# Optimization experiments

Measured on AMD Instinct MI355X. Metric: run time of the kernel, lower is better.

Reference implementation:

```python
import jax, jax.numpy as jnp
import numpy as np

B, D, P, K_ROUTE = 131072, 256, 16, 4


def setup_inputs() -> dict:
    key = jax.random.key(0)
    ks = jax.random.split(key, 12)
    w_scale = 0.02
    return {
        "z_n": jax.random.normal(ks[0], (B, D), dtype=jnp.float32),
        "z_sea": jax.random.normal(ks[1], (B, D), dtype=jnp.float32),
        "z_trend": jax.random.normal(ks[2], (B, D), dtype=jnp.float32),
        "noise_z": jax.random.normal(ks[3], (B, D), dtype=jnp.float32),   # randn_like(z_fused)
        "noise_r": jax.random.normal(ks[4], (B, P), dtype=jnp.float32),   # randn_like(routing_logits)
        "patch_candidates": jax.random.randint(ks[5], (P,), 1, 64, dtype=jnp.int32),
        "W_proj": jax.random.normal(ks[6], (D, 3 * D), dtype=jnp.float32) * w_scale,
        "b_proj": jnp.zeros((D,), dtype=jnp.float32),
        "W_route": jax.random.normal(ks[7], (P, D), dtype=jnp.float32) * w_scale,
        "b_route": jnp.zeros((P,), dtype=jnp.float32),
        "W_noise": jax.random.normal(ks[8], (P, D), dtype=jnp.float32) * w_scale,
        "b_noise": jnp.zeros((P,), dtype=jnp.float32),
    }


def reference(z_n, z_sea, z_trend, noise_z, noise_r, patch_candidates,
              W_proj, b_proj, W_route, b_route, W_noise, b_noise):
    # feature fusion: Linear(3D -> D) on concat
    z_concat = jnp.concatenate([z_n, z_sea, z_trend], axis=-1)        # [B, 3D]
    z_fused = z_concat @ W_proj.T + b_proj                            # [B, D]
    gating_input = z_fused + noise_z * 0.1                            # noise injection 1
    routing_logits = gating_input @ W_route.T + b_route               # [B, P]
    noise_scale = jax.nn.softplus(gating_input @ W_noise.T + b_noise)  # [B, P]
    routing_logits = routing_logits + noise_r * noise_scale           # noise injection 2
    routing_weights = jax.nn.softmax(routing_logits, axis=-1)         # [B, P]
    top_k_values, top_k_indices = jax.lax.top_k(routing_weights, K_ROUTE)  # [B, K]
    rows = jnp.arange(routing_weights.shape[0])[:, None]
    sparse_routing = jnp.zeros_like(routing_weights).at[rows, top_k_indices].set(top_k_values)
    selected_patches = patch_candidates[top_k_indices]                # [B, K]
    return (sparse_routing, selected_patches, top_k_indices)
```

## Files before the change

kernel.cpp:

```cpp
#include <hip/hip_runtime.h>
#include <math.h>

#define B_ROWS 131072
#define ROWS 128
#define XP 36
#define MP 36
#define LP 34

__global__ void precompute_M(const float* __restrict__ Wp,
                             const float* __restrict__ Wr,
                             const float* __restrict__ Wn,
                             const float* __restrict__ bp,
                             const float* __restrict__ br,
                             const float* __restrict__ bn,
                             float* __restrict__ M,
                             float* __restrict__ c) {
  int o = blockIdx.x * 256 + threadIdx.x;
  if (o < 32 * 1024) {
    int j = o >> 10, k = o & 1023;
    const float* W = (j < 16) ? Wr : Wn;
    int jj = j & 15;
    float v;
    if (k < 768) {
      double s = 0.0;
      for (int d = 0; d < 256; ++d)
        s += (double)W[jj * 256 + d] * (double)Wp[d * 768 + k];
      v = (float)s;
    } else {
      v = 0.1f * W[jj * 256 + (k - 768)];
    }
    M[o] = v;
  }
  if (blockIdx.x == 0 && threadIdx.x < 32) {
    int j = threadIdx.x, jj = j & 15;
    const float* W = (j < 16) ? Wr : Wn;
    const float* b = (j < 16) ? br : bn;
    double s = (double)b[jj];
    for (int d = 0; d < 256; ++d)
      s += (double)W[jj * 256 + d] * (double)bp[d];
    c[j] = (float)s;
  }
}

__global__ __launch_bounds__(256, 3)
void router_main(const float* __restrict__ zn, const float* __restrict__ zs,
                 const float* __restrict__ zt, const float* __restrict__ nz,
                 const float* __restrict__ nr, const int* __restrict__ patches,
                 const float* __restrict__ M, const float* __restrict__ c,
                 float* __restrict__ out) {
  __shared__ float Xs[ROWS * XP];
  __shared__ float Ms[32 * MP];
  __shared__ float Ls[ROWS * LP];
  const int t = threadIdx.x;
  const int row0 = blockIdx.x * ROWS;
  const int jg = t & 7;
  const int rg = t >> 3;
  const int sr = t >> 3;
  const int sk4 = t & 7;

  float accf[4][4];
  double accd[4][4];
#pragma unroll
  for (int a = 0; a < 4; ++a)
#pragma unroll
    for (int b = 0; b < 4; ++b) { accf[a][b] = 0.f; accd[a][b] = 0.0; }

  for (int s = 0; s < 32; ++s) {
    const int k0 = s * 32;
    const float* src; int col0;
    if (k0 < 256)      { src = zn; col0 = k0; }
    else if (k0 < 512) { src = zs; col0 = k0 - 256; }
    else if (k0 < 768) { src = zt; col0 = k0 - 512; }
    else               { src = nz; col0 = k0 - 768; }

    float4 xg[4];
#pragma unroll
    for (int i = 0; i < 4; ++i)
      xg[i] = *(const float4*)&src[(size_t)(row0 + sr + 32 * i) * 256 + col0 + 4 * sk4];
    float4 mg = *(const float4*)&M[(size_t)(t >> 3) * 1024 + k0 + 4 * sk4];

    __syncthreads();
#pragma unroll
    for (int i = 0; i < 4; ++i)
      *(float4*)&Xs[(sr + 32 * i) * XP + 4 * sk4] = xg[i];
    *(float4*)&Ms[(t >> 3) * MP + 4 * sk4] = mg;
    __syncthreads();

#pragma unroll
    for (int ks = 0; ks < 8; ++ks) {
      const int k = 4 * ks;
      float4 m4[4], x4[4];
#pragma unroll
      for (int jj = 0; jj < 4; ++jj)
        m4[jj] = *(const float4*)&Ms[(jg + 8 * jj) * MP + k];
#pragma unroll
      for (int rr = 0; rr < 4; ++rr)
        x4[rr] = *(const float4*)&Xs[(rg + 32 * rr) * XP + k];
#pragma unroll
      for (int jj = 0; jj < 4; ++jj)
#pragma unroll
        for (int rr = 0; rr < 4; ++rr) {
          accf[jj][rr] += m4[jj].x * x4[rr].x;
          accf[jj][rr] += m4[jj].y * x4[rr].y;
          accf[jj][rr] += m4[jj].z * x4[rr].z;
          accf[jj][rr] += m4[jj].w * x4[rr].w;
        }
    }
#pragma unroll
    for (int jj = 0; jj < 4; ++jj)
#pragma unroll
      for (int rr = 0; rr < 4; ++rr) { accd[jj][rr] += (double)accf[jj][rr]; accf[jj][rr] = 0.f; }
  }

#pragma unroll
  for (int jj = 0; jj < 4; ++jj) {
    const int j = jg + 8 * jj;
    const float cj = c[j];
#pragma unroll
    for (int rr = 0; rr < 4; ++rr) {
      const int r = rg + 32 * rr;
      Ls[r * LP + j] = (float)(accd[jj][rr] + (double)cj);
    }
  }
  __syncthreads();

  if (t < ROWS) {
    const int row = row0 + t;
    float L[32];
#pragma unroll
    for (int j = 0; j < 32; ++j) L[j] = Ls[t * LP + j];

    float nrv[16];
#pragma unroll
    for (int q = 0; q < 4; ++q) {
      float4 v = *(const float4*)&nr[(size_t)row * 16 + 4 * q];
      nrv[4 * q] = v.x; nrv[4 * q + 1] = v.y; nrv[4 * q + 2] = v.z; nrv[4 * q + 3] = v.w;
    }

    float lg[16];
#pragma unroll
    for (int p = 0; p < 16; ++p) {
      const float x = L[16 + p];
      const float sp = (x > 15.f) ? x : log1pf(expf(x));
      lg[p] = L[p] + nrv[p] * sp;
    }

    float mx = lg[0];
#pragma unroll
    for (int p = 1; p < 16; ++p) mx = fmaxf(mx, lg[p]);
    float e[16]; float sum = 0.f;
#pragma unroll
    for (int p = 0; p < 16; ++p) { e[p] = expf(lg[p] - mx); sum += e[p]; }
    float w[16];
#pragma unroll
    for (int p = 0; p < 16; ++p) w[p] = e[p] / sum;

    int idx[4]; float val[4]; unsigned used = 0;
#pragma unroll
    for (int kk = 0; kk < 4; ++kk) {
      float best = -1.f; int bi = 0;
#pragma unroll
      for (int p = 0; p < 16; ++p) {
        const bool ok = (((used >> p) & 1u) == 0u) && (w[p] > best);
        best = ok ? w[p] : best;
        bi = ok ? p : bi;
      }
      idx[kk] = bi; val[kk] = best; used |= (1u << bi);
    }

    float so[16];
#pragma unroll
    for (int p = 0; p < 16; ++p) {
      float v = 0.f;
#pragma unroll
      for (int kk = 0; kk < 4; ++kk) v = (idx[kk] == p) ? val[kk] : v;
      so[p] = v;
    }
#pragma unroll
    for (int q = 0; q < 4; ++q)
      *(float4*)&out[(size_t)row * 16 + 4 * q] =
          make_float4(so[4 * q], so[4 * q + 1], so[4 * q + 2], so[4 * q + 3]);

    float4 pv, iv;
    pv.x = (float)patches[idx[0]]; pv.y = (float)patches[idx[1]];
    pv.z = (float)patches[idx[2]]; pv.w = (float)patches[idx[3]];
    iv.x = (float)idx[0]; iv.y = (float)idx[1];
    iv.z = (float)idx[2]; iv.w = (float)idx[3];
    *(float4*)&out[(size_t)B_ROWS * 16 + (size_t)row * 4] = pv;
    *(float4*)&out[(size_t)B_ROWS * 20 + (size_t)row * 4] = iv;
  }
}

extern "C" void kernel_launch(void* const* d_in, const int* in_sizes, int n_in,
                              void* d_out, int out_size, void* d_ws, size_t ws_size,
                              hipStream_t stream) {
  const float* zn = (const float*)d_in[0];
  const float* zs = (const float*)d_in[1];
  const float* zt = (const float*)d_in[2];
  const float* nz = (const float*)d_in[3];
  const float* nr = (const float*)d_in[4];
  const int*   pc = (const int*)d_in[5];
  const float* Wp = (const float*)d_in[6];
  const float* bp = (const float*)d_in[7];
  const float* Wr = (const float*)d_in[8];
  const float* br = (const float*)d_in[9];
  const float* Wn = (const float*)d_in[10];
  const float* bn = (const float*)d_in[11];
  float* out = (float*)d_out;
  float* M = (float*)d_ws;
  float* c = M + 32 * 1024;

  precompute_M<<<128, 256, 0, stream>>>(Wp, Wr, Wn, bp, br, bn, M, c);
  router_main<<<B_ROWS / ROWS, 256, 0, stream>>>(zn, zs, zt, nz, nr, pc, M, c, out);
}
```

Before: 602.2 us.

## Give each thread one row with all 32 outputs, reading transposed M uniformly

The weight matrix is now stored transposed so that each k row holds 32 contiguous outputs. Each thread owns a whole input row and all 32 accumulators, and reads M with wave-uniform addresses, which should turn into scalar or broadcast loads in place of the LDS tile of M. This removes the M staging in shared memory, the Ls round trip and the idle half of the block in the epilogue, and doubles rows per block to 256. In exchange it raises register pressure (32 float plus 32 double accumulators) and lowers occupancy, and each thread reads Xs at a stride of 36 floats, which may cause LDS bank conflicts.

```diff
diff --git a/kernel.cpp b/kernel.cpp
--- a/kernel.cpp
+++ b/kernel.cpp
@@ -2,19 +2,17 @@
 #include <math.h>
 
 #define B_ROWS 131072
-#define ROWS 128
+#define ROWS 256
 #define XP 36
-#define MP 36
-#define LP 34
 
-__global__ void precompute_M(const float* __restrict__ Wp,
-                             const float* __restrict__ Wr,
-                             const float* __restrict__ Wn,
-                             const float* __restrict__ bp,
-                             const float* __restrict__ br,
-                             const float* __restrict__ bn,
-                             float* __restrict__ M,
-                             float* __restrict__ c) {
+__global__ void precompute_Mt(const float* __restrict__ Wp,
+                              const float* __restrict__ Wr,
+                              const float* __restrict__ Wn,
+                              const float* __restrict__ bp,
+                              const float* __restrict__ br,
+                              const float* __restrict__ bn,
+                              float* __restrict__ Mt,
+                              float* __restrict__ c) {
   int o = blockIdx.x * 256 + threadIdx.x;
   if (o < 32 * 1024) {
     int j = o >> 10, k = o & 1023;
@@ -29,7 +27,7 @@
     } else {
       v = 0.1f * W[jj * 256 + (k - 768)];
     }
-    M[o] = v;
+    Mt[k * 32 + j] = v;
   }
   if (blockIdx.x == 0 && threadIdx.x < 32) {
     int j = threadIdx.x, jj = j & 15;
@@ -42,28 +40,22 @@
   }
 }
 
-__global__ __launch_bounds__(256, 3)
+__global__ __launch_bounds__(256, 2)
 void router_main(const float* __restrict__ zn, const float* __restrict__ zs,
                  const float* __restrict__ zt, const float* __restrict__ nz,
                  const float* __restrict__ nr, const int* __restrict__ patches,
-                 const float* __restrict__ M, const float* __restrict__ c,
+                 const float* __restrict__ Mt, const float* __restrict__ c,
                  float* __restrict__ out) {
   __shared__ float Xs[ROWS * XP];
-  __shared__ float Ms[32 * MP];
-  __shared__ float Ls[ROWS * LP];
   const int t = threadIdx.x;
   const int row0 = blockIdx.x * ROWS;
-  const int jg = t & 7;
-  const int rg = t >> 3;
   const int sr = t >> 3;
   const int sk4 = t & 7;
 
-  float accf[4][4];
-  double accd[4][4];
+  float  accf[32];
+  double accd[32];
 #pragma unroll
-  for (int a = 0; a < 4; ++a)
-#pragma unroll
-    for (int b = 0; b < 4; ++b) { accf[a][b] = 0.f; accd[a][b] = 0.0; }
+  for (int j = 0; j < 32; ++j) { accf[j] = 0.f; accd[j] = 0.0; }
 
   for (int s = 0; s < 32; ++s) {
     const int k0 = s * 32;
@@ -73,122 +65,97 @@
     else if (k0 < 768) { src = zt; col0 = k0 - 512; }
     else               { src = nz; col0 = k0 - 768; }
 
-    float4 xg[4];
+    float4 xg[8];
 #pragma unroll
-    for (int i = 0; i < 4; ++i)
+    for (int i = 0; i < 8; ++i)
       xg[i] = *(const float4*)&src[(size_t)(row0 + sr + 32 * i) * 256 + col0 + 4 * sk4];
-    float4 mg = *(const float4*)&M[(size_t)(t >> 3) * 1024 + k0 + 4 * sk4];
 
     __syncthreads();
 #pragma unroll
-    for (int i = 0; i < 4; ++i)
+    for (int i = 0; i < 8; ++i)
       *(float4*)&Xs[(sr + 32 * i) * XP + 4 * sk4] = xg[i];
-    *(float4*)&Ms[(t >> 3) * MP + 4 * sk4] = mg;
     __syncthreads();
 
 #pragma unroll
     for (int ks = 0; ks < 8; ++ks) {
-      const int k = 4 * ks;
-      float4 m4[4], x4[4];
+      const float4 x4 = *(const float4*)&Xs[t * XP + 4 * ks];
+      const int kb = k0 + 4 * ks;
 #pragma unroll
-      for (int jj = 0; jj < 4; ++jj)
-        m4[jj] = *(const float4*)&Ms[(jg + 8 * jj) * MP + k];
+      for (int kk = 0; kk < 4; ++kk) {
+        const float xk = (kk == 0) ? x4.x : (kk == 1) ? x4.y : (kk == 2) ? x4.z : x4.w;
+        const float* mrow = &Mt[(size_t)(kb + kk) * 32];
 #pragma unroll
-      for (int rr = 0; rr < 4; ++rr)
-        x4[rr] = *(const float4*)&Xs[(rg + 32 * rr) * XP + k];
-#pragma unroll
-      for (int jj = 0; jj < 4; ++jj)
-#pragma unroll
-        for (int rr = 0; rr < 4; ++rr) {
-          accf[jj][rr] += m4[jj].x * x4[rr].x;
-          accf[jj][rr] += m4[jj].y * x4[rr].y;
-          accf[jj][rr] += m4[jj].z * x4[rr].z;
-          accf[jj][rr] += m4[jj].w * x4[rr].w;
-        }
+        for (int j = 0; j < 32; ++j)
+          accf[j] += mrow[j] * xk;
+      }
     }
 #pragma unroll
-    for (int jj = 0; jj < 4; ++jj)
-#pragma unroll
-      for (int rr = 0; rr < 4; ++rr) { accd[jj][rr] += (double)accf[jj][rr]; accf[jj][rr] = 0.f; }
+    for (int j = 0; j < 32; ++j) { accd[j] += (double)accf[j]; accf[j] = 0.f; }
   }
 
+  const int row = row0 + t;
+  float L[32];
 #pragma unroll
-  for (int jj = 0; jj < 4; ++jj) {
-    const int j = jg + 8 * jj;
-    const float cj = c[j];
+  for (int j = 0; j < 32; ++j) L[j] = (float)(accd[j] + (double)c[j]);
+
+  float nrv[16];
 #pragma unroll
-    for (int rr = 0; rr < 4; ++rr) {
-      const int r = rg + 32 * rr;
-      Ls[r * LP + j] = (float)(accd[jj][rr] + (double)cj);
-    }
+  for (int q = 0; q < 4; ++q) {
+    float4 v = *(const float4*)&nr[(size_t)row * 16 + 4 * q];
+    nrv[4 * q] = v.x; nrv[4 * q + 1] = v.y; nrv[4 * q + 2] = v.z; nrv[4 * q + 3] = v.w;
   }
-  __syncthreads();
 
-  if (t < ROWS) {
-    const int row = row0 + t;
-    float L[32];
+  float lg[16];
 #pragma unroll
-    for (int j = 0; j < 32; ++j) L[j] = Ls[t * LP + j];
+  for (int p = 0; p < 16; ++p) {
+    const float x = L[16 + p];
+    const float sp = (x > 15.f) ? x : log1pf(expf(x));
+    lg[p] = L[p] + nrv[p] * sp;
+  }
 
-    float nrv[16];
+  float mx = lg[0];
 #pragma unroll
-    for (int q = 0; q < 4; ++q) {
-      float4 v = *(const float4*)&nr[(size_t)row * 16 + 4 * q];
-      nrv[4 * q] = v.x; nrv[4 * q + 1] = v.y; nrv[4 * q + 2] = v.z; nrv[4 * q + 3] = v.w;
-    }
+  for (int p = 1; p < 16; ++p) mx = fmaxf(mx, lg[p]);
+  float e[16]; float sum = 0.f;
+#pragma unroll
+  for (int p = 0; p < 16; ++p) { e[p] = expf(lg[p] - mx); sum += e[p]; }
+  float w[16];
+#pragma unroll
+  for (int p = 0; p < 16; ++p) w[p] = e[p] / sum;
 
-    float lg[16];
+  int idx[4]; float val[4]; unsigned used = 0;
+#pragma unroll
+  for (int kk = 0; kk < 4; ++kk) {
+    float best = -1.f; int bi = 0;
 #pragma unroll
     for (int p = 0; p < 16; ++p) {
-      const float x = L[16 + p];
-      const float sp = (x > 15.f) ? x : log1pf(expf(x));
-      lg[p] = L[p] + nrv[p] * sp;
+      const bool ok = (((used >> p) & 1u) == 0u) && (w[p] > best);
+      best = ok ? w[p] : best;
+      bi = ok ? p : bi;
     }
+    idx[kk] = bi; val[kk] = best; used |= (1u << bi);
+  }
 
-    float mx = lg[0];
+  float so[16];
 #pragma unroll
-    for (int p = 1; p < 16; ++p) mx = fmaxf(mx, lg[p]);
-    float e[16]; float sum = 0.f;
+  for (int p = 0; p < 16; ++p) {
+    float v = 0.f;
 #pragma unroll
-    for (int p = 0; p < 16; ++p) { e[p] = expf(lg[p] - mx); sum += e[p]; }
-    float w[16];
+    for (int kk = 0; kk < 4; ++kk) v = (idx[kk] == p) ? val[kk] : v;
+    so[p] = v;
+  }
 #pragma unroll
-    for (int p = 0; p < 16; ++p) w[p] = e[p] / sum;
+  for (int q = 0; q < 4; ++q)
+    *(float4*)&out[(size_t)row * 16 + 4 * q] =
+        make_float4(so[4 * q], so[4 * q + 1], so[4 * q + 2], so[4 * q + 3]);
 
-    int idx[4]; float val[4]; unsigned used = 0;
-#pragma unroll
-    for (int kk = 0; kk < 4; ++kk) {
-      float best = -1.f; int bi = 0;
-#pragma unroll
-      for (int p = 0; p < 16; ++p) {
-        const bool ok = (((used >> p) & 1u) == 0u) && (w[p] > best);
-        best = ok ? w[p] : best;
-        bi = ok ? p : bi;
-      }
-      idx[kk] = bi; val[kk] = best; used |= (1u << bi);
-    }
-
-    float so[16];
-#pragma unroll
-    for (int p = 0; p < 16; ++p) {
-      float v = 0.f;
-#pragma unroll
-      for (int kk = 0; kk < 4; ++kk) v = (idx[kk] == p) ? val[kk] : v;
-      so[p] = v;
-    }
-#pragma unroll
-    for (int q = 0; q < 4; ++q)
-      *(float4*)&out[(size_t)row * 16 + 4 * q] =
-          make_float4(so[4 * q], so[4 * q + 1], so[4 * q + 2], so[4 * q + 3]);
-
-    float4 pv, iv;
-    pv.x = (float)patches[idx[0]]; pv.y = (float)patches[idx[1]];
-    pv.z = (float)patches[idx[2]]; pv.w = (float)patches[idx[3]];
-    iv.x = (float)idx[0]; iv.y = (float)idx[1];
-    iv.z = (float)idx[2]; iv.w = (float)idx[3];
-    *(float4*)&out[(size_t)B_ROWS * 16 + (size_t)row * 4] = pv;
-    *(float4*)&out[(size_t)B_ROWS * 20 + (size_t)row * 4] = iv;
-  }
+  float4 pv, iv;
+  pv.x = (float)patches[idx[0]]; pv.y = (float)patches[idx[1]];
+  pv.z = (float)patches[idx[2]]; pv.w = (float)patches[idx[3]];
+  iv.x = (float)idx[0]; iv.y = (float)idx[1];
+  iv.z = (float)idx[2]; iv.w = (float)idx[3];
+  *(float4*)&out[(size_t)B_ROWS * 16 + (size_t)row * 4] = pv;
+  *(float4*)&out[(size_t)B_ROWS * 20 + (size_t)row * 4] = iv;
 }
 
 extern "C" void kernel_launch(void* const* d_in, const int* in_sizes, int n_in,
@@ -207,9 +174,9 @@
   const float* Wn = (const float*)d_in[10];
   const float* bn = (const float*)d_in[11];
   float* out = (float*)d_out;
-  float* M = (float*)d_ws;
-  float* c = M + 32 * 1024;
+  float* Mt = (float*)d_ws;
+  float* c  = Mt + 1024 * 32;
 
-  precompute_M<<<128, 256, 0, stream>>>(Wp, Wr, Wn, bp, br, bn, M, c);
-  router_main<<<B_ROWS / ROWS, 256, 0, stream>>>(zn, zs, zt, nz, nr, pc, M, c, out);
+  precompute_Mt<<<128, 256, 0, stream>>>(Wp, Wr, Wn, bp, br, bn, Mt, c);
+  router_main<<<B_ROWS / ROWS, 256, 0, stream>>>(zn, zs, zt, nz, nr, pc, Mt, c, out);
 }
```

Result: slower. 781.2 us (+29.7%).
